# Kernel tuning notes

Hardware: AMD Instinct MI355X
Metric: run time of the kernel (lower is better)

Reference implementation:

```python
import jax, jax.numpy as jnp
import numpy as np

B, N, K, M = 4, 32768, 128, 1024
C_IN, C_OUT, C_ATT, H = 256, 256, 256, 8
G = 32  # GroupNorm groups
EPS = 1e-6


def heat_diffusion(x, mass, evals, evecs, t):
    # to_basis: evecs^T @ (mass * x)  -> [B,K,C]
    x_spec = jnp.einsum('bnk,bnc->bkc', evecs, x * mass[..., None])
    coefs = jnp.exp(-evals[..., None] * t[None, None, :])  # [B,K,C]
    # from_basis: evecs @ spec -> [B,N,C]
    return jnp.einsum('bnk,bkc->bnc', evecs, coefs * x_spec)


def setup_inputs() -> dict:
    key = jax.random.key(0)
    ks = jax.random.split(key, 16)
    x = jax.random.normal(ks[0], (B, N, C_IN), jnp.float32)
    mass = jax.random.uniform(ks[1], (B, N), jnp.float32, 0.1, 1.0)
    evals = jnp.sort(jax.random.uniform(ks[2], (B, K), jnp.float32, 0.0, 10.0), axis=-1)
    evecs = jax.random.normal(ks[3], (B, N, K), jnp.float32) / np.sqrt(N)
    # unique sorted farthest-point indices per mesh (equiv. to boolean mask with M True)
    far_idx = jnp.stack([jnp.sort(jax.random.permutation(jax.random.fold_in(ks[4], b), N)[:M])
                         for b in range(B)]).astype(jnp.int32)
    s = 1.0 / np.sqrt(C_IN)
    params = dict(
        diff_in_t=jnp.full((C_IN,), 0.01, jnp.float32),
        diff_out_t=jnp.full((C_OUT,), 0.01, jnp.float32),
        gn_w=jnp.ones((C_IN,), jnp.float32),
        gn_b=jnp.zeros((C_IN,), jnp.float32),
        Wq=jax.random.normal(ks[5], (C_IN, C_ATT), jnp.float32) * s,
        bq=jnp.zeros((C_ATT,), jnp.float32),
        Wk=jax.random.normal(ks[6], (C_IN, C_ATT), jnp.float32) * s,
        bk=jnp.zeros((C_ATT,), jnp.float32),
        Wv=jax.random.normal(ks[7], (C_IN, C_ATT), jnp.float32) * s,
        bv=jnp.zeros((C_ATT,), jnp.float32),
        Wo=jax.random.normal(ks[8], (C_ATT, C_OUT), jnp.float32) * s,
        bo=jnp.zeros((C_OUT,), jnp.float32),
        out_w=jnp.ones((C_OUT,), jnp.float32),
    )
    return dict(x=x, mass=mass, evals=evals, evecs=evecs, far_idx=far_idx, **params)


def reference(x, mass, evals, evecs, far_idx, diff_in_t, diff_out_t, gn_w, gn_b,
              Wq, bq, Wk, bk, Wv, bv, Wo, bo, out_w):
    # clamp (torch does this in-place under no_grad)
    diff_in_t = jnp.maximum(diff_in_t, 1e-8)
    diff_out_t = jnp.maximum(diff_out_t, 1e-8)
    out_w = jnp.maximum(out_w, 1e-8)

    x = heat_diffusion(x, mass, evals, evecs, diff_in_t)  # [B,N,C_IN]

    # masked gather of farthest points -> [B,M,C_IN]
    x_far = jnp.take_along_axis(x, far_idx[..., None], axis=1)

    # GroupNorm over (group-channels, points)
    xg = x_far.reshape(B, M, G, C_IN // G)
    mu = jnp.mean(xg, axis=(1, 3), keepdims=True)
    var = jnp.var(xg, axis=(1, 3), keepdims=True)
    xg = (xg - mu) * jax.lax.rsqrt(var + EPS)
    x_far = xg.reshape(B, M, C_IN) * gn_w + gn_b

    d = C_ATT // H
    q = (x_far @ Wq + bq).reshape(B, M, H, d)
    k = (x_far @ Wk + bk).reshape(B, M, H, d)
    v = (x_far @ Wv + bv).reshape(B, M, H, d)
    scores = jnp.einsum('bqhd,bkhd->bhqk', q, k) / np.sqrt(d)
    attn = jax.nn.softmax(scores, axis=-1)
    x_far = jnp.einsum('bhqk,bkhd->bqhd', attn, v).reshape(B, M, C_ATT)
    x_far = x_far @ Wo + bo  # [B,M,C_OUT]

    # scatter back into zeros at the farthest-point rows
    z = jnp.zeros((B, N, C_OUT), x.dtype)
    z = z.at[jnp.arange(B)[:, None], far_idx].set(x_far)

    out = heat_diffusion(z, mass, evals, evecs, diff_out_t)
    return out * out_w[None, None, :]
```

## Files before the change

kernel.cpp:

```cpp
#include <hip/hip_runtime.h>
#include <hip/hip_bf16.h>


#define Bn 4
#define Nn 32768
#define Kn 128
#define Cn 256
#define Mn 1024
#define Hn 8
#define Dn 32
#define NCH 64
#define MCH 16

typedef _Float16 f16;
typedef _Float16 f16x8 __attribute__((ext_vector_type(8)));
typedef float f32x4 __attribute__((ext_vector_type(4)));
typedef unsigned int u32;
typedef unsigned int u32x4 __attribute__((ext_vector_type(4)));

__device__ __forceinline__ void gload_lds16(const float* g, float* l) {
    __builtin_amdgcn_global_load_lds(
        (const __attribute__((address_space(1))) void*)g,
        (__attribute__((address_space(3))) void*)l, 16, 0, 0);
}

static __device__ __forceinline__ u32 packf16(f16 a, f16 b) {
    union { f16 h[2]; u32 u; } x;
    x.h[0] = a; x.h[1] = b;
    return x.u;
}

__global__ __launch_bounds__(512) void k_tobasis1(
    const float* __restrict__ x, const float* __restrict__ mass,
    const float* __restrict__ evecs, float* __restrict__ part)
{
    const int nch = blockIdx.x, b = blockIdx.z;
    const int n0 = nch * (Nn / NCH);
    const int t = threadIdx.x;
    const int lane = t & 63, w = t >> 6;
    const int lr = lane & 15, lg = lane >> 4;
    const int wm = (w & 1) * 64;
    const int wc = (w >> 1) * 64;

    __shared__ __align__(16) float evS[2][32][128];
    __shared__ __align__(16) float xS[2][32][256];
    __shared__ __align__(16) f16 evT[128][64];
    __shared__ __align__(16) f16 xT[256][64];
    __shared__ __align__(16) float massS[512];

    const size_t rb0 = (size_t)b * Nn + n0;
    const float* ebase = evecs + rb0 * Kn;
    const float* xbase = x + rb0 * Cn;

    f32x4 acc[4][4] = {};

    if (w < 2) gload_lds16(mass + rb0 + w * 256 + lane * 4, massS + w * 256);
#pragma unroll
    for (int ss = 0; ss < 2; ss++) {
        const float* eb = ebase + (size_t)ss * 32 * Kn;
        const float* xb = xbase + (size_t)ss * 32 * Cn;
#pragma unroll
        for (int iw = 0; iw < 2; iw++)
            gload_lds16(eb + (w * 2 + iw) * 256 + lane * 4, &evS[ss][0][0] + (w * 2 + iw) * 256);
#pragma unroll
        for (int iw = 0; iw < 4; iw++)
            gload_lds16(xb + (w * 4 + iw) * 256 + lane * 4, &xS[ss][0][0] + (w * 4 + iw) * 256);
    }

    for (int s = 0; s < 16; s++) {
        const int p = s & 1;
        if (s == 15) { asm volatile("s_waitcnt vmcnt(0)" ::: "memory"); }
        else         { asm volatile("s_waitcnt vmcnt(6)" ::: "memory"); }
        __builtin_amdgcn_sched_barrier(0);
        __builtin_amdgcn_s_barrier();

        {
            const int k = t & 127;
            const int g = t >> 7;
            f16x8 hv, lv;
#pragma unroll
            for (int r = 0; r < 8; r++) {
                const float f = evS[p][g * 8 + r][k];
                const f16 h = (f16)f;
                hv[r] = h;
                lv[r] = (f16)(f - (float)h);
            }
            *(f16x8*)&evT[k][((g) ^ (k & 7)) * 8] = hv;
            *(f16x8*)&evT[k][((4 + g) ^ (k & 7)) * 8] = lv;
        }
        {
            const int c = t & 255;
            const int g2 = t >> 8;
#pragma unroll
            for (int jj = 0; jj < 2; jj++) {
                const int ch = g2 * 2 + jj;
                f16x8 hv, lv;
#pragma unroll
                for (int r = 0; r < 8; r++) {
                    const int n = ch * 8 + r;
                    const float f = xS[p][n][c] * massS[s * 32 + n];
                    const f16 h = (f16)f;
                    hv[r] = h;
                    lv[r] = (f16)(f - (float)h);
                }
                *(f16x8*)&xT[c][((ch) ^ (c & 7)) * 8] = hv;
                *(f16x8*)&xT[c][((4 + ch) ^ (c & 7)) * 8] = lv;
            }
        }

        asm volatile("s_waitcnt lgkmcnt(0)" ::: "memory");
        __builtin_amdgcn_sched_barrier(0);
        __builtin_amdgcn_s_barrier();

        if (s + 2 < 16) {
            const float* eb = ebase + (size_t)(s + 2) * 32 * Kn;
            const float* xb = xbase + (size_t)(s + 2) * 32 * Cn;
#pragma unroll
            for (int iw = 0; iw < 2; iw++)
                gload_lds16(eb + (w * 2 + iw) * 256 + lane * 4, &evS[p][0][0] + (w * 2 + iw) * 256);
#pragma unroll
            for (int iw = 0; iw < 4; iw++)
                gload_lds16(xb + (w * 4 + iw) * 256 + lane * 4, &xS[p][0][0] + (w * 4 + iw) * 256);
        }

        f16x8 aH[4], aL[4], bH[4], bL[4];
#pragma unroll
        for (int i = 0; i < 4; i++) {
            const int rk = wm + i * 16 + lr;
            aH[i] = *(const f16x8*)&evT[rk][((lg) ^ (rk & 7)) * 8];
            aL[i] = *(const f16x8*)&evT[rk][((4 + lg) ^ (rk & 7)) * 8];
            const int rc = wc + i * 16 + lr;
            bH[i] = *(const f16x8*)&xT[rc][((lg) ^ (rc & 7)) * 8];
            bL[i] = *(const f16x8*)&xT[rc][((4 + lg) ^ (rc & 7)) * 8];
        }
#pragma unroll
        for (int i = 0; i < 4; i++)
#pragma unroll
            for (int j = 0; j < 4; j++) {
                acc[i][j] = __builtin_amdgcn_mfma_f32_16x16x32_f16(aH[i], bH[j], acc[i][j], 0, 0, 0);
                acc[i][j] = __builtin_amdgcn_mfma_f32_16x16x32_f16(aH[i], bL[j], acc[i][j], 0, 0, 0);
                acc[i][j] = __builtin_amdgcn_mfma_f32_16x16x32_f16(aL[i], bH[j], acc[i][j], 0, 0, 0);
            }
    }

    float* dst = part + ((size_t)b * NCH + nch) * (Kn * Cn);
#pragma unroll
    for (int i = 0; i < 4; i++)
#pragma unroll
        for (int j = 0; j < 4; j++) {
            const int m0 = wm + i * 16 + lg * 4;
            const int c = wc + j * 16 + lr;
#pragma unroll
            for (int r = 0; r < 4; r++)
                dst[(size_t)(m0 + r) * Cn + c] = acc[i][j][r];
        }
}

__global__ __launch_bounds__(256) void k_reduce(
    const float* __restrict__ part, int nchunks,
    const float* __restrict__ evals, const float* __restrict__ tvec,
    float* __restrict__ spec)
{
    const int b = blockIdx.x >> 7, k = blockIdx.x & 127, c = threadIdx.x;
    float ssum = 0.f;
    const float* p = part + ((size_t)b * nchunks * Kn + k) * Cn + c;
    for (int j = 0; j < nchunks; j++) ssum += p[(size_t)j * Kn * Cn];
    const float lam = evals[b * Kn + k];
    const float tt = fmaxf(tvec[c], 1e-8f);
    spec[((size_t)b * Kn + k) * Cn + c] = ssum * __expf(-lam * tt);
}

__global__ __launch_bounds__(256) void k_spectr(
    const float* __restrict__ spec, f16* __restrict__ sTh, f16* __restrict__ sTl)
{
    const int kc = blockIdx.x, b = blockIdx.y;
    const int t = threadIdx.x;
    __shared__ f16 lh[32][258];
    __shared__ f16 ll[32][258];
#pragma unroll 8
    for (int k2 = 0; k2 < 32; k2++) {
        const float f = spec[((size_t)b * Kn + kc * 32 + k2) * Cn + t];
        const f16 h = (f16)f;
        lh[k2][t] = h;
        ll[k2][t] = (f16)(f - (float)h);
    }
    __syncthreads();
    f16x8 vh[4], vl[4];
#pragma unroll
    for (int q = 0; q < 4; q++)
#pragma unroll
        for (int j = 0; j < 8; j++) { vh[q][j] = lh[q * 8 + j][t]; vl[q][j] = ll[q * 8 + j][t]; }
    f16* dh = sTh + ((size_t)b * 256 + t) * Kn + kc * 32;
    f16* dl = sTl + ((size_t)b * 256 + t) * Kn + kc * 32;
#pragma unroll
    for (int q = 0; q < 4; q++) {
        *(f16x8*)(dh + q * 8) = vh[q];
        *(f16x8*)(dl + q * 8) = vl[q];
    }
}

__global__ __launch_bounds__(128) void k_gather(
    const float* __restrict__ evecs, const float* __restrict__ mass,
    const int* __restrict__ far, float* __restrict__ evf, float* __restrict__ massf)
{
    const int row = blockIdx.x;
    const int b = row >> 10;
    const int idx = far[row];
    const int t = threadIdx.x;
    evf[(size_t)row * Kn + t] = evecs[((size_t)b * Nn + idx) * Kn + t];
    if (t == 0) massf[row] = mass[(size_t)b * Nn + idx];
}

struct G3 {
    const float* W[3];
    const float* bias[3];
    float* out[3];
};

template<int KD, bool PERB, bool MMASS>
__global__ __launch_bounds__(256) void k_gemm64(
    const float* __restrict__ X, G3 g, const float* __restrict__ massf)
{
    const int mt = blockIdx.x, ct = blockIdx.y, z = blockIdx.z;
    const int row0 = mt * 64, c0 = ct * 64;
    const int b = row0 >> 10;
    const float* Wp = g.W[z];
    const float* bias = g.bias[z];
    float* out = g.out[z];
    const size_t woff = PERB ? (size_t)b * KD * 256 : 0;

    __shared__ float xT[32][68];
    __shared__ float wl[32][64];
    const int t = threadIdx.x, tx = t & 15, ty = t >> 4;
    float acc[4][4] = {};

    for (int k0 = 0; k0 < KD; k0 += 32) {
        {
            const int m = t >> 2, cc0 = (t & 3) * 8;
            const float* xs = X + (size_t)(row0 + m) * KD + k0 + cc0;
            float4 a0 = *(const float4*)xs, a1 = *(const float4*)(xs + 4);
            xT[cc0 + 0][m] = a0.x; xT[cc0 + 1][m] = a0.y; xT[cc0 + 2][m] = a0.z; xT[cc0 + 3][m] = a0.w;
            xT[cc0 + 4][m] = a1.x; xT[cc0 + 5][m] = a1.y; xT[cc0 + 6][m] = a1.z; xT[cc0 + 7][m] = a1.w;
        }
        {
            const int cc = t >> 3, col = (t & 7) * 8;
            const float* wsrc = Wp + woff + (size_t)(k0 + cc) * 256 + c0 + col;
            float4 a0 = *(const float4*)wsrc, a1 = *(const float4*)(wsrc + 4);
            wl[cc][col + 0] = a0.x; wl[cc][col + 1] = a0.y; wl[cc][col + 2] = a0.z; wl[cc][col + 3] = a0.w;
            wl[cc][col + 4] = a1.x; wl[cc][col + 5] = a1.y; wl[cc][col + 6] = a1.z; wl[cc][col + 7] = a1.w;
        }
        __syncthreads();
#pragma unroll 8
        for (int cc = 0; cc < 32; cc++) {
            float4 xv = *(const float4*)&xT[cc][ty * 4];
            float4 wv = *(const float4*)&wl[cc][tx * 4];
            float xa[4] = {xv.x, xv.y, xv.z, xv.w};
            float wa[4] = {wv.x, wv.y, wv.z, wv.w};
#pragma unroll
            for (int i = 0; i < 4; i++)
#pragma unroll
                for (int j = 0; j < 4; j++) acc[i][j] += xa[i] * wa[j];
        }
        __syncthreads();
    }
    float bj[4] = {0.f, 0.f, 0.f, 0.f};
    if (bias) {
#pragma unroll
        for (int j = 0; j < 4; j++) bj[j] = bias[c0 + tx * 4 + j];
    }
#pragma unroll
    for (int i = 0; i < 4; i++) {
        const int row = row0 + ty * 4 + i;
        const float mm = MMASS ? massf[row] : 1.f;
        *(float4*)(out + (size_t)row * 256 + c0 + tx * 4) =
            make_float4((acc[i][0] + bj[0]) * mm, (acc[i][1] + bj[1]) * mm,
                        (acc[i][2] + bj[2]) * mm, (acc[i][3] + bj[3]) * mm);
    }
}

__global__ __launch_bounds__(256) void k_gnstats(const float* __restrict__ xfar, float* __restrict__ gst)
{
    const int b = blockIdx.x >> 5, g = blockIdx.x & 31;
    const int t = threadIdx.x;
    float s = 0.f, s2 = 0.f;
#pragma unroll
    for (int i = 0; i < 4; i++) {
        const int m = t * 4 + i;
        const float* p = xfar + ((size_t)b * Mn + m) * Cn + g * 8;
        float4 a = *(const float4*)p;
        float4 c = *(const float4*)(p + 4);
        s += a.x + a.y + a.z + a.w + c.x + c.y + c.z + c.w;
        s2 += a.x * a.x + a.y * a.y + a.z * a.z + a.w * a.w +
              c.x * c.x + c.y * c.y + c.z * c.z + c.w * c.w;
    }
    __shared__ float sb[256], sb2[256];
    sb[t] = s; sb2[t] = s2;
    __syncthreads();
    for (int o = 128; o > 0; o >>= 1) {
        if (t < o) { sb[t] += sb[t + o]; sb2[t] += sb2[t + o]; }
        __syncthreads();
    }
    if (t == 0) {
        const float mean = sb[0] * (1.f / 8192.f);
        const float var = sb2[0] * (1.f / 8192.f) - mean * mean;
        gst[2 * blockIdx.x] = mean;
        gst[2 * blockIdx.x + 1] = rsqrtf(var + 1e-6f);
    }
}

__global__ __launch_bounds__(256) void k_gnapply(
    const float* __restrict__ xfar, const float* __restrict__ gst,
    const float* __restrict__ gw, const float* __restrict__ gb, float* __restrict__ xn)
{
    const int idx = (blockIdx.x * 256 + threadIdx.x) * 4;
    const int c = idx & 255;
    const int row = idx >> 8;
    const int b = row >> 10;
    const int g = c >> 3;
    const float2 st = *(const float2*)&gst[2 * (b * 32 + g)];
    float4 vv = *(const float4*)&xfar[idx];
    float4 w4 = *(const float4*)&gw[c];
    float4 b4 = *(const float4*)&gb[c];
    float4 o;
    o.x = (vv.x - st.x) * st.y * w4.x + b4.x;
    o.y = (vv.y - st.x) * st.y * w4.y + b4.y;
    o.z = (vv.z - st.x) * st.y * w4.z + b4.z;
    o.w = (vv.w - st.x) * st.y * w4.w + b4.w;
    *(float4*)&xn[idx] = o;
}

__global__ __launch_bounds__(256) void k_attn(
    const float* __restrict__ q, const float* __restrict__ kbuf, const float* __restrict__ vbuf,
    float* __restrict__ att)
{
    const int qt = blockIdx.x;
    const int bh = blockIdx.y;
    const int b = bh >> 3, h = bh & 7;
    const int t = threadIdx.x;
    const int lane = t & 63, w = t >> 6;
    const int lr = lane & 15, lg = lane >> 4;

    __shared__ __align__(16) f16 Kh[64][32];
    __shared__ __align__(16) f16 Kl[64][32];
    __shared__ __align__(16) f16 Vh[32][64];
    __shared__ __align__(16) f16 Vl[32][64];
    __shared__ __align__(16) u32 Pw[4][16][68];

    const size_t base = (size_t)b * Mn * Cn + h * Dn;
    const int q0 = qt * 64;

    f16x8 Qh, Ql;
    {
        const float* qp = q + base + (size_t)(q0 + w * 16 + lr) * Cn + lg * 8;
        f32x4 a0 = *(const f32x4*)qp;
        f32x4 a1 = *(const f32x4*)(qp + 4);
        const float scale = 0.17677669529663687f;
        float qv[8] = {a0[0], a0[1], a0[2], a0[3], a1[0], a1[1], a1[2], a1[3]};
#pragma unroll
        for (int r = 0; r < 8; r++) {
            const float f = qv[r] * scale;
            const f16 hh = (f16)f;
            Qh[r] = hh;
            Ql[r] = (f16)(f - (float)hh);
        }
    }

    const int krow = t >> 2, kdg = (t & 3) * 8;
    const int vrow = (t & 31) * 2, vdc = (t >> 5) * 4;

    f32x4 kr0, kr1, va, vb;
    {
        const float* kp = kbuf + base + (size_t)krow * Cn + kdg;
        kr0 = *(const f32x4*)kp; kr1 = *(const f32x4*)(kp + 4);
        const float* vp = vbuf + base + (size_t)vrow * Cn + vdc;
        va = *(const f32x4*)vp; vb = *(const f32x4*)(vp + Cn);
    }

    float m_i[4], l_i[4];
    f32x4 acc[2] = {};
#pragma unroll
    for (int r = 0; r < 4; r++) { m_i[r] = -1e30f; l_i[r] = 0.f; }

#pragma unroll 1
    for (int kt = 0; kt < 16; kt++) {
        asm volatile("" ::: "memory");
        __builtin_amdgcn_s_barrier();

        {
            float kv[8] = {kr0[0], kr0[1], kr0[2], kr0[3], kr1[0], kr1[1], kr1[2], kr1[3]};
            f16x8 hv, lv;
#pragma unroll
            for (int r = 0; r < 8; r++) {
                const f16 hh = (f16)kv[r];
                hv[r] = hh;
                lv[r] = (f16)(kv[r] - (float)hh);
            }
            *(f16x8*)&Kh[krow][kdg] = hv;
            *(f16x8*)&Kl[krow][kdg] = lv;
        }
        {
            float v0[4] = {va[0], va[1], va[2], va[3]};
            float v1[4] = {vb[0], vb[1], vb[2], vb[3]};
#pragma unroll
            for (int j = 0; j < 4; j++) {
                const int d = vdc + j;
                const f16 h0 = (f16)v0[j], h1 = (f16)v1[j];
                const f16 l0 = (f16)(v0[j] - (float)h0), l1 = (f16)(v1[j] - (float)h1);
                const int col = vrow >> 1;
                const int idx = (((col >> 2) ^ (d & 7)) << 2) | (col & 3);
                ((u32*)&Vh[d][0])[idx] = packf16(h0, h1);
                ((u32*)&Vl[d][0])[idx] = packf16(l0, l1);
            }
        }
        if (kt < 15) {
            const float* kp = kbuf + base + (size_t)((kt + 1) * 64 + krow) * Cn + kdg;
            kr0 = *(const f32x4*)kp; kr1 = *(const f32x4*)(kp + 4);
            const float* vp = vbuf + base + (size_t)((kt + 1) * 64 + vrow) * Cn + vdc;
            va = *(const f32x4*)vp; vb = *(const f32x4*)(vp + Cn);
        }

        asm volatile("s_waitcnt lgkmcnt(0)" ::: "memory");
        __builtin_amdgcn_sched_barrier(0);
        __builtin_amdgcn_s_barrier();

        f32x4 s[4];
#pragma unroll
        for (int ct = 0; ct < 4; ct++) {
            const f16x8 khi = *(const f16x8*)&Kh[ct * 16 + lr][lg * 8];
            const f16x8 klo = *(const f16x8*)&Kl[ct * 16 + lr][lg * 8];
            f32x4 z = {};
            z = __builtin_amdgcn_mfma_f32_16x16x32_f16(Qh, khi, z, 0, 0, 0);
            z = __builtin_amdgcn_mfma_f32_16x16x32_f16(Qh, klo, z, 0, 0, 0);
            z = __builtin_amdgcn_mfma_f32_16x16x32_f16(Ql, khi, z, 0, 0, 0);
            s[ct] = z;
        }

        float tm[4];
#pragma unroll
        for (int r = 0; r < 4; r++)
            tm[r] = fmaxf(fmaxf(s[0][r], s[1][r]), fmaxf(s[2][r], s[3][r]));
#pragma unroll
        for (int r = 0; r < 4; r++) {
            tm[r] = fmaxf(tm[r], __shfl_xor(tm[r], 1));
            tm[r] = fmaxf(tm[r], __shfl_xor(tm[r], 2));
            tm[r] = fmaxf(tm[r], __shfl_xor(tm[r], 4));
            tm[r] = fmaxf(tm[r], __shfl_xor(tm[r], 8));
        }
        float corr[4], rs[4];
#pragma unroll
        for (int r = 0; r < 4; r++) {
            const float nm = fmaxf(m_i[r], tm[r]);
            corr[r] = __expf(m_i[r] - nm);
            m_i[r] = nm;
            rs[r] = 0.f;
        }
#pragma unroll
        for (int ct = 0; ct < 4; ct++)
#pragma unroll
            for (int r = 0; r < 4; r++) {
                const float p = __expf(s[ct][r] - m_i[r]);
                rs[r] += p;
                const f16 ph = (f16)p;
                const f16 pl = (f16)(p - (float)ph);
                Pw[w][lg * 4 + r][ct * 16 + lr] = packf16(ph, pl);
            }
#pragma unroll
        for (int r = 0; r < 4; r++) {
            rs[r] += __shfl_xor(rs[r], 1);
            rs[r] += __shfl_xor(rs[r], 2);
            rs[r] += __shfl_xor(rs[r], 4);
            rs[r] += __shfl_xor(rs[r], 8);
            l_i[r] = l_i[r] * corr[r] + rs[r];
        }
#pragma unroll
        for (int dt = 0; dt < 2; dt++)
#pragma unroll
            for (int r = 0; r < 4; r++) acc[dt][r] *= corr[r];

        asm volatile("s_waitcnt lgkmcnt(0)" ::: "memory");
        __builtin_amdgcn_sched_barrier(0);

        f16x8 pah[2], pal[2];
#pragma unroll
        for (int kc = 0; kc < 2; kc++) {
            const u32* prow = &Pw[w][lr][0] + kc * 32 + lg * 8;
            u32x4 ua = *(const u32x4*)prow;
            u32x4 ub = *(const u32x4*)(prow + 4);
            union { u32 wd[4]; f16x8 v; } hh, ll;
            hh.wd[0] = __builtin_amdgcn_perm(ua[1], ua[0], 0x05040100u);
            hh.wd[1] = __builtin_amdgcn_perm(ua[3], ua[2], 0x05040100u);
            hh.wd[2] = __builtin_amdgcn_perm(ub[1], ub[0], 0x05040100u);
            hh.wd[3] = __builtin_amdgcn_perm(ub[3], ub[2], 0x05040100u);
            ll.wd[0] = __builtin_amdgcn_perm(ua[1], ua[0], 0x07060302u);
            ll.wd[1] = __builtin_amdgcn_perm(ua[3], ua[2], 0x07060302u);
            ll.wd[2] = __builtin_amdgcn_perm(ub[1], ub[0], 0x07060302u);
            ll.wd[3] = __builtin_amdgcn_perm(ub[3], ub[2], 0x07060302u);
            pah[kc] = hh.v;
            pal[kc] = ll.v;
        }

#pragma unroll
        for (int dt = 0; dt < 2; dt++)
#pragma unroll
            for (int kc = 0; kc < 2; kc++) {
                const int d = dt * 16 + lr;
                const int ch = ((kc * 4 + lg) ^ (lr & 7)) * 8;
                const f16x8 vh = *(const f16x8*)&Vh[d][ch];
                const f16x8 vl = *(const f16x8*)&Vl[d][ch];
                acc[dt] = __builtin_amdgcn_mfma_f32_16x16x32_f16(pah[kc], vh, acc[dt], 0, 0, 0);
                acc[dt] = __builtin_amdgcn_mfma_f32_16x16x32_f16(pah[kc], vl, acc[dt], 0, 0, 0);
                acc[dt] = __builtin_amdgcn_mfma_f32_16x16x32_f16(pal[kc], vh, acc[dt], 0, 0, 0);
            }
    }

#pragma unroll
    for (int r = 0; r < 4; r++) {
        const float inv = 1.f / l_i[r];
        const size_t orow = (size_t)b * Mn + q0 + w * 16 + lg * 4 + r;
#pragma unroll
        for (int dt = 0; dt < 2; dt++)
            att[orow * Cn + h * Dn + dt * 16 + lr] = acc[dt][r] * inv;
    }
}

__global__ __launch_bounds__(256) void k_tobasis2(
    const float* __restrict__ evf, const float* __restrict__ xo, float* __restrict__ part)
{
    const int mch = blockIdx.x, ct = blockIdx.y, b = blockIdx.z;
    const int m0 = mch * (Mn / MCH);
    const int c0 = ct * 128;
    __shared__ float ev[32][128];
    __shared__ float xm[32][128];
    const int t = threadIdx.x, tx = t & 15, ty = t >> 4;
    float acc[8][8];
#pragma unroll
    for (int i = 0; i < 8; i++)
#pragma unroll
        for (int j = 0; j < 8; j++) acc[i][j] = 0.f;
    const int lr = t >> 3, lc = (t & 7) * 16;
    for (int s = 0; s < Mn / MCH; s += 32) {
        const size_t mrow = (size_t)b * Mn + m0 + s + lr;
        {
            const float* es = evf + mrow * Kn + lc;
            *(float4*)&ev[lr][lc]      = *(const float4*)es;
            *(float4*)&ev[lr][lc + 4]  = *(const float4*)(es + 4);
            *(float4*)&ev[lr][lc + 8]  = *(const float4*)(es + 8);
            *(float4*)&ev[lr][lc + 12] = *(const float4*)(es + 12);
            const float* xs = xo + mrow * Cn + c0 + lc;
            *(float4*)&xm[lr][lc]      = *(const float4*)xs;
            *(float4*)&xm[lr][lc + 4]  = *(const float4*)(xs + 4);
            *(float4*)&xm[lr][lc + 8]  = *(const float4*)(xs + 8);
            *(float4*)&xm[lr][lc + 12] = *(const float4*)(xs + 12);
        }
        __syncthreads();
#pragma unroll 4
        for (int nn = 0; nn < 32; nn++) {
            float4 e0 = *(const float4*)&ev[nn][ty * 4];
            float4 e1 = *(const float4*)&ev[nn][64 + ty * 4];
            float4 x0 = *(const float4*)&xm[nn][tx * 4];
            float4 x1 = *(const float4*)&xm[nn][64 + tx * 4];
            float ee[8] = {e0.x, e0.y, e0.z, e0.w, e1.x, e1.y, e1.z, e1.w};
            float xx[8] = {x0.x, x0.y, x0.z, x0.w, x1.x, x1.y, x1.z, x1.w};
#pragma unroll
            for (int i = 0; i < 8; i++)
#pragma unroll
                for (int j = 0; j < 8; j++) acc[i][j] += ee[i] * xx[j];
        }
        __syncthreads();
    }
    float* dst = part + ((size_t)b * MCH + mch) * (Kn * Cn);
#pragma unroll
    for (int i = 0; i < 8; i++) {
        const int k = (i < 4) ? (ty * 4 + i) : (64 + ty * 4 + i - 4);
        *(float4*)(dst + (size_t)k * Cn + c0 + tx * 4) =
            make_float4(acc[i][0], acc[i][1], acc[i][2], acc[i][3]);
        *(float4*)(dst + (size_t)k * Cn + c0 + 64 + tx * 4) =
            make_float4(acc[i][4], acc[i][5], acc[i][6], acc[i][7]);
    }
}

__global__ __launch_bounds__(512) void k_frombasis2(
    const float* __restrict__ evecs, const f16* __restrict__ sTh,
    const f16* __restrict__ sTl, const float* __restrict__ outw,
    float* __restrict__ out)
{
    const int nt = blockIdx.x, b = blockIdx.z;
    const int n0 = nt * 128;
    const int t = threadIdx.x;
    const int lane = t & 63, w = t >> 6;
    const int lr = lane & 15, lg = lane >> 4;
    const int wn = (w & 1) * 64;
    const int wc = (w >> 1) * 64;

    const float* Abase = evecs + ((size_t)b * Nn + n0 + wn + lr) * Kn + lg * 8;
    const f16* Bh = sTh + ((size_t)(b * 256 + wc + lr)) * Kn + lg * 8;
    const f16* Bl = sTl + ((size_t)(b * 256 + wc + lr)) * Kn + lg * 8;

    f32x4 acc[4][4] = {};

#pragma unroll
    for (int kk = 0; kk < 4; kk++) {
        f16x8 bh[4], bl[4];
#pragma unroll
        for (int cf = 0; cf < 4; cf++) {
            bh[cf] = *(const f16x8*)(Bh + (size_t)cf * 16 * Kn + kk * 32);
            bl[cf] = *(const f16x8*)(Bl + (size_t)cf * 16 * Kn + kk * 32);
        }
#pragma unroll
        for (int rf = 0; rf < 4; rf++) {
            const float* ap = Abase + (size_t)rf * 16 * Kn + kk * 32;
            f32x4 a0 = *(const f32x4*)ap;
            f32x4 a1 = *(const f32x4*)(ap + 4);
            float av[8] = {a0[0], a0[1], a0[2], a0[3], a1[0], a1[1], a1[2], a1[3]};
            f16x8 ah, al;
#pragma unroll
            for (int r = 0; r < 8; r++) {
                const float f = av[r] * 256.f;
                const f16 hh = (f16)f;
                ah[r] = hh;
                al[r] = (f16)(f - (float)hh);
            }
#pragma unroll
            for (int cf = 0; cf < 4; cf++) {
                acc[rf][cf] = __builtin_amdgcn_mfma_f32_16x16x32_f16(ah, bh[cf], acc[rf][cf], 0, 0, 0);
                acc[rf][cf] = __builtin_amdgcn_mfma_f32_16x16x32_f16(ah, bl[cf], acc[rf][cf], 0, 0, 0);
                acc[rf][cf] = __builtin_amdgcn_mfma_f32_16x16x32_f16(al, bh[cf], acc[rf][cf], 0, 0, 0);
            }
        }
    }

    float ow4[4];
#pragma unroll
    for (int cf = 0; cf < 4; cf++)
        ow4[cf] = fmaxf(outw[wc + cf * 16 + lr], 1e-8f) * (1.f / 256.f);
#pragma unroll
    for (int rf = 0; rf < 4; rf++)
#pragma unroll
        for (int cf = 0; cf < 4; cf++) {
            const int nn = n0 + wn + rf * 16 + lg * 4;
            const int c = wc + cf * 16 + lr;
#pragma unroll
            for (int r = 0; r < 4; r++)
                out[((size_t)b * Nn + nn + r) * Cn + c] = acc[rf][cf][r] * ow4[cf];
        }
}

extern "C" void kernel_launch(void* const* d_in, const int* in_sizes, int n_in,
                              void* d_out, int out_size, void* d_ws, size_t ws_size,
                              hipStream_t stream)
{
    const float* x     = (const float*)d_in[0];
    const float* mass  = (const float*)d_in[1];
    const float* evals = (const float*)d_in[2];
    const float* evecs = (const float*)d_in[3];
    const int*   far   = (const int*)d_in[4];
    const float* t_in  = (const float*)d_in[5];
    const float* t_out = (const float*)d_in[6];
    const float* gn_w  = (const float*)d_in[7];
    const float* gn_b  = (const float*)d_in[8];
    const float* Wq    = (const float*)d_in[9];
    const float* bq    = (const float*)d_in[10];
    const float* Wk    = (const float*)d_in[11];
    const float* bk    = (const float*)d_in[12];
    const float* Wv    = (const float*)d_in[13];
    const float* bv    = (const float*)d_in[14];
    const float* Wo    = (const float*)d_in[15];
    const float* bo    = (const float*)d_in[16];
    const float* outw  = (const float*)d_in[17];
    float* out = (float*)d_out;
    float* ws = (float*)d_ws;

    float* A     = ws;
    float* evf   = ws    + 8388608;
    float* massf = evf   + 524288;
    float* gst   = massf + 4096;
    float* pm    = gst   + 256;
    float* pl    = pm    + 262144;
    float* spec1 = pl    + 262144;
    float* xfar  = spec1 + 131072;
    float* xn    = xfar  + 1048576;
    float* q     = xn    + 1048576;
    float* kk    = q     + 1048576;
    float* v     = kk    + 1048576;
    float* part2 = A;
    float* spec2 = spec1;
    float* xo    = xfar;
    float* att   = xn;
    f16* specTh  = (f16*)pm;
    f16* specTl  = specTh + 131072;
    (void)pl;

    k_tobasis1<<<dim3(NCH, 1, Bn), 512, 0, stream>>>(x, mass, evecs, A);
    k_reduce<<<Bn * Kn, Cn, 0, stream>>>(A, NCH, evals, t_in, spec1);
    k_gather<<<Bn * Mn, Kn, 0, stream>>>(evecs, mass, far, evf, massf);
    {
        G3 g{};
        g.W[0] = spec1; g.bias[0] = nullptr; g.out[0] = xfar;
        k_gemm64<128, true, false><<<dim3(64, 4, 1), 256, 0, stream>>>(evf, g, nullptr);
    }
    k_gnstats<<<Bn * 32, 256, 0, stream>>>(xfar, gst);
    k_gnapply<<<1024, 256, 0, stream>>>(xfar, gst, gn_w, gn_b, xn);
    {
        G3 g{};
        g.W[0] = Wq; g.W[1] = Wk; g.W[2] = Wv;
        g.bias[0] = bq; g.bias[1] = bk; g.bias[2] = bv;
        g.out[0] = q; g.out[1] = kk; g.out[2] = v;
        k_gemm64<256, false, false><<<dim3(64, 4, 3), 256, 0, stream>>>(xn, g, nullptr);
    }
    k_attn<<<dim3(16, 32), 256, 0, stream>>>(q, kk, v, att);
    {
        G3 g{};
        g.W[0] = Wo; g.bias[0] = bo; g.out[0] = xo;
        k_gemm64<256, false, true><<<dim3(64, 4, 1), 256, 0, stream>>>(att, g, massf);
    }
    k_tobasis2<<<dim3(MCH, 2, Bn), 256, 0, stream>>>(evf, xo, part2);
    k_reduce<<<Bn * Kn, Cn, 0, stream>>>(part2, MCH, evals, t_out, spec2);
    k_spectr<<<dim3(4, Bn), 256, 0, stream>>>(spec2, specTh, specTl);
    k_frombasis2<<<dim3(256, 1, Bn), 512, 0, stream>>>(evecs, specTh, specTl, outw, out);
}
```

Measured before the change: 533.0 us.

## Stage split-f16 evecs tile in LDS shared across waves in frombasis

In k_frombasis2, each of the 8 waves previously loaded and split its own evecs rows into hi/lo f16, so each row was loaded and converted by 4 waves. Now every thread converts one 8-element chunk per k-step and writes hi and lo into a double-buffered, XOR-swizzled LDS tile, and the waves read their MFMA A fragments from LDS. The next k-step's global load is issued before the barrier to overlap latency. The cost is a workgroup barrier per k-step and 32KB of LDS, with the k loop no longer unrolled.

```diff
diff --git a/kernel.cpp b/kernel.cpp
--- a/kernel.cpp
+++ b/kernel.cpp
@@ -592,34 +592,56 @@
     const int wn = (w & 1) * 64;
     const int wc = (w >> 1) * 64;
 
-    const float* Abase = evecs + ((size_t)b * Nn + n0 + wn + lr) * Kn + lg * 8;
-    const f16* Bh = sTh + ((size_t)(b * 256 + wc + lr)) * Kn + lg * 8;
-    const f16* Bl = sTl + ((size_t)(b * 256 + wc + lr)) * Kn + lg * 8;
+    __shared__ __align__(16) f16 aT[2][128][64];
+
+    const int srow = t >> 2;
+    const int skc = t & 3;
+    const float* Abase = evecs + ((size_t)b * Nn + n0 + srow) * Kn + skc * 8;
+
+    const f16* Bh = sTh + ((size_t)b * 256 + wc + lr) * Kn + lg * 8;
+    const f16* Bl = sTl + ((size_t)b * 256 + wc + lr) * Kn + lg * 8;
 
     f32x4 acc[4][4] = {};
 
-#pragma unroll
+    f32x4 a0 = *(const f32x4*)(Abase);
+    f32x4 a1 = *(const f32x4*)(Abase + 4);
+
+#pragma unroll 1
     for (int kk = 0; kk < 4; kk++) {
+        const int p = kk & 1;
+        {
+            float av[8] = {a0[0], a0[1], a0[2], a0[3], a1[0], a1[1], a1[2], a1[3]};
+            f16x8 hv, lv;
+#pragma unroll
+            for (int r = 0; r < 8; r++) {
+                const float f = av[r] * 256.f;
+                const f16 hh = (f16)f;
+                hv[r] = hh;
+                lv[r] = (f16)(f - (float)hh);
+            }
+            *(f16x8*)&aT[p][srow][((skc) ^ (srow & 7)) * 8] = hv;
+            *(f16x8*)&aT[p][srow][((4 + skc) ^ (srow & 7)) * 8] = lv;
+        }
+        if (kk < 3) {
+            a0 = *(const f32x4*)(Abase + (kk + 1) * 32);
+            a1 = *(const f32x4*)(Abase + (kk + 1) * 32 + 4);
+        }
         f16x8 bh[4], bl[4];
 #pragma unroll
         for (int cf = 0; cf < 4; cf++) {
             bh[cf] = *(const f16x8*)(Bh + (size_t)cf * 16 * Kn + kk * 32);
             bl[cf] = *(const f16x8*)(Bl + (size_t)cf * 16 * Kn + kk * 32);
         }
+
+        asm volatile("s_waitcnt lgkmcnt(0)" ::: "memory");
+        __builtin_amdgcn_sched_barrier(0);
+        __builtin_amdgcn_s_barrier();
+
 #pragma unroll
         for (int rf = 0; rf < 4; rf++) {
-            const float* ap = Abase + (size_t)rf * 16 * Kn + kk * 32;
-            f32x4 a0 = *(const f32x4*)ap;
-            f32x4 a1 = *(const f32x4*)(ap + 4);
-            float av[8] = {a0[0], a0[1], a0[2], a0[3], a1[0], a1[1], a1[2], a1[3]};
-            f16x8 ah, al;
-#pragma unroll
-            for (int r = 0; r < 8; r++) {
-                const float f = av[r] * 256.f;
-                const f16 hh = (f16)f;
-                ah[r] = hh;
-                al[r] = (f16)(f - (float)hh);
-            }
+            const int rn = wn + rf * 16 + lr;
+            const f16x8 ah = *(const f16x8*)&aT[p][rn][((lg) ^ (rn & 7)) * 8];
+            const f16x8 al = *(const f16x8*)&aT[p][rn][((4 + lg) ^ (rn & 7)) * 8];
 #pragma unroll
             for (int cf = 0; cf < 4; cf++) {
                 acc[rf][cf] = __builtin_amdgcn_mfma_f32_16x16x32_f16(ah, bh[cf], acc[rf][cf], 0, 0, 0);
```

After: 506.2 us. -5.0%, faster.
